# Performance work log

Hardware: AMD Instinct MI355X
Metric: run time of the kernel (lower is better)

## Reference

```python
import jax, jax.numpy as jnp
import numpy as np

N_NODES = 100000
N_EDGES = 1600000
F_IN = 64
HEADS = 4
F_OUT = 16
NEG_SLOPE = 0.2


def setup_inputs() -> dict:
    key = jax.random.key(0)
    k1, k2, k3, k4, k5 = jax.random.split(key, 5)
    x = jax.random.normal(k1, (N_NODES, F_IN), dtype=jnp.float32)
    edge_index = jax.random.randint(k2, (2, N_EDGES), 0, N_NODES, dtype=jnp.int64)
    # Glorot-ish scaled params
    W = jax.random.normal(k3, (HEADS, F_IN, F_OUT), dtype=jnp.float32) / np.sqrt(F_IN)
    a_src = jax.random.normal(k4, (HEADS, F_OUT), dtype=jnp.float32) / np.sqrt(F_OUT)
    a_dst = jax.random.normal(k5, (HEADS, F_OUT), dtype=jnp.float32) / np.sqrt(F_OUT)
    bias = jnp.zeros((HEADS * F_OUT,), dtype=jnp.float32)
    return {"x": x, "edge_index": edge_index, "W": W, "a_src": a_src,
            "a_dst": a_dst, "bias": bias}


def reference(x, edge_index, W, a_src, a_dst, bias):
    """Graph-attention conv (GAT-style) over a point-cloud graph.

    x: [N, F_in] node features; edge_index: [2, E] (src, dst);
    W: [H, F_in, F_out]; a_src/a_dst: [H, F_out]; bias: [H*F_out].
    Returns [N, H*F_out].
    """
    N = x.shape[0]
    src, dst = edge_index[0], edge_index[1]

    # Per-head linear projection: [N, H, F_out]
    h = jnp.einsum('nf,hfo->nho', x, W)

    # Per-node attention logits (decomposed GAT form): [N, H]
    logit_s = jnp.einsum('nho,ho->nh', h, a_src)
    logit_d = jnp.einsum('nho,ho->nh', h, a_dst)

    # Per-edge raw attention: [E, H]
    e = jax.nn.leaky_relu(logit_s[src] + logit_d[dst], negative_slope=NEG_SLOPE)

    # Segment softmax over incoming edges of each dst node
    m = jax.ops.segment_max(e, dst, num_segments=N)        # [N, H]
    m = jax.lax.stop_gradient(m)                           # softmax shift invariance
    e_exp = jnp.exp(e - m[dst])                            # [E, H]
    denom = jax.ops.segment_sum(e_exp, dst, num_segments=N)  # [N, H]
    alpha = e_exp / (denom[dst] + 1e-16)                   # [E, H]

    # Weighted message aggregation: scatter-add to dst
    msg = h[src] * alpha[:, :, None]                       # [E, H, F_out]
    out = jax.ops.segment_sum(msg, dst, num_segments=N)    # [N, H, F_out]

    return out.reshape(N, -1) + bias
```

## Files before the change

### kernel.cpp

```cpp
#include <hip/hip_runtime.h>

constexpr int N_NODES_C = 100000;
constexpr int N_EDGES_C = 1600000;
constexpr int F_IN_C = 64;
constexpr int HEADS_C = 4;
constexpr int F_OUT_C = 16;
constexpr float NEG_SLOPE_C = 0.2f;

constexpr int BUCK_SHIFT = 8;
constexpr int BUCK_NODES = 1 << BUCK_SHIFT;
constexpr int NBUCK = (N_NODES_C + BUCK_NODES - 1) / BUCK_NODES;
constexpr int BUCK_CAP = 5120;
constexpr int PART_BLOCKS = 256;
constexpr int EDGES_PER_PART_BLOCK = (N_EDGES_C + PART_BLOCKS - 1) / PART_BLOCKS;

typedef __attribute__((ext_vector_type(8))) short short8v;
typedef __attribute__((ext_vector_type(4))) float f32x4;

static __device__ __forceinline__ unsigned short f2bf(float f)
{
    const unsigned u = __float_as_uint(f);
    return (unsigned short)((u + 0x7FFF + ((u >> 16) & 1)) >> 16);
}
static __device__ __forceinline__ float bf2f(unsigned short b)
{
    return __uint_as_float(((unsigned)b) << 16);
}

__global__ __launch_bounds__(256) void k_prep(
    const float* __restrict__ W, const float* __restrict__ a_src,
    const float* __restrict__ a_dst, int* __restrict__ bucket_cursor,
    unsigned short* __restrict__ Bpack, unsigned short* __restrict__ Bpack2)
{
    __shared__ float sW[HEADS_C * F_IN_C * F_OUT_C];
    __shared__ float sA[2 * HEADS_C * F_OUT_C];
    const int t = threadIdx.x;
    for (int i = t; i < NBUCK; i += 256) bucket_cursor[i] = 0;
    for (int i = t; i < HEADS_C * F_IN_C * F_OUT_C; i += 256) sW[i] = W[i];
    if (t < HEADS_C * F_OUT_C) { sA[t] = a_src[t]; sA[64 + t] = a_dst[t]; }
    __syncthreads();

    for (int idx = t; idx < 4096; idx += 256) {
        const int j    = idx & 7;
        const int lane = (idx >> 3) & 63;
        const int nt   = (idx >> 9) & 3;
        const int kc   = (idx >> 11) & 1;
        const int col  = nt * 16 + (lane & 15);
        const int k    = kc * 32 + (lane >> 4) * 8 + j;
        Bpack[idx] = f2bf(sW[(col >> 4) * 1024 + k * 16 + (col & 15)]);
    }
    for (int idx = t; idx < 1024; idx += 256) {
        const int j    = idx & 7;
        const int lane = (idx >> 3) & 63;
        const int kc   = (idx >> 9) & 1;
        const int col  = lane & 15;
        const int k    = kc * 32 + (lane >> 4) * 8 + j;
        float v = 0.f;
        if (col < 8) {
            const int hd = col & 3;
            const float* wrow = &sW[hd * 1024 + k * 16];
            const float* av   = &sA[(col < 4 ? 0 : 64) + hd * 16];
            #pragma unroll
            for (int o = 0; o < 16; ++o) v = fmaf(wrow[o], av[o], v);
        }
        Bpack2[idx] = f2bf(v);
    }
}

__global__ __launch_bounds__(256) void k_project(
    const float* __restrict__ x, const unsigned short* __restrict__ Bpack,
    const unsigned short* __restrict__ Bpack2,
    unsigned short* __restrict__ h, float* __restrict__ ls, float* __restrict__ ld)
{
    const int wid  = threadIdx.x >> 6;
    const int lane = threadIdx.x & 63;
    const int node0 = (blockIdx.x * 4 + wid) * 16;
    const int colg = lane & 15;
    const int kg   = lane >> 4;

    const int rowc = min(node0 + colg, N_NODES_C - 1);
    short8v afrag[2];
    #pragma unroll
    for (int kc = 0; kc < 2; ++kc) {
        const float4* xp = (const float4*)&x[(size_t)rowc * 64 + kc * 32 + kg * 8];
        const float4 q0 = xp[0];
        const float4 q1 = xp[1];
        afrag[kc][0] = (short)f2bf(q0.x); afrag[kc][1] = (short)f2bf(q0.y);
        afrag[kc][2] = (short)f2bf(q0.z); afrag[kc][3] = (short)f2bf(q0.w);
        afrag[kc][4] = (short)f2bf(q1.x); afrag[kc][5] = (short)f2bf(q1.y);
        afrag[kc][6] = (short)f2bf(q1.z); afrag[kc][7] = (short)f2bf(q1.w);
    }

    f32x4 acc[4] = {{0.f,0.f,0.f,0.f},{0.f,0.f,0.f,0.f},
                    {0.f,0.f,0.f,0.f},{0.f,0.f,0.f,0.f}};
    f32x4 accL = {0.f,0.f,0.f,0.f};
    #pragma unroll
    for (int kc = 0; kc < 2; ++kc) {
        #pragma unroll
        for (int nt = 0; nt < 4; ++nt) {
            const short8v bfrag = *(const short8v*)&Bpack[((kc * 4 + nt) * 64 + lane) * 8];
            acc[nt] = __builtin_amdgcn_mfma_f32_16x16x32_bf16(afrag[kc], bfrag, acc[nt], 0, 0, 0);
        }
        const short8v bfrag2 = *(const short8v*)&Bpack2[(kc * 64 + lane) * 8];
        accL = __builtin_amdgcn_mfma_f32_16x16x32_bf16(afrag[kc], bfrag2, accL, 0, 0, 0);
    }

    #pragma unroll
    for (int nt = 0; nt < 4; ++nt) {
        #pragma unroll
        for (int i = 0; i < 4; ++i) {
            const int node = node0 + kg * 4 + i;
            if (node < N_NODES_C)
                h[(size_t)node * 64 + nt * 16 + colg] = f2bf(acc[nt][i]);
        }
    }
    #pragma unroll
    for (int i = 0; i < 4; ++i) {
        const int node = node0 + kg * 4 + i;
        if (node < N_NODES_C) {
            if (colg < 4)      ls[node * HEADS_C + colg]       = accL[i];
            else if (colg < 8) ld[node * HEADS_C + (colg - 4)] = accL[i];
        }
    }
}

__global__ __launch_bounds__(1024) void k_partition(
    const int* __restrict__ src, const int* __restrict__ dst,
    int* __restrict__ bucket_cursor, int* __restrict__ bucketed)
{
    __shared__ int cnt[NBUCK];
    __shared__ int base[NBUCK];
    __shared__ unsigned spack[EDGES_PER_PART_BLOCK];
    __shared__ unsigned short sbuck[EDGES_PER_PART_BLOCK];
    const int t = threadIdx.x;
    for (int i = t; i < NBUCK; i += 1024) cnt[i] = 0;
    __syncthreads();
    const int e0 = blockIdx.x * EDGES_PER_PART_BLOCK;
    const int nE = min(EDGES_PER_PART_BLOCK, N_EDGES_C - e0);
    for (int e = t; e < nE; e += 1024) {
        const int d = dst[e0 + e];
        const int b = d >> BUCK_SHIFT;
        spack[e] = (unsigned)src[e0 + e] | ((unsigned)(d & (BUCK_NODES - 1)) << 17);
        sbuck[e] = (unsigned short)b;
        atomicAdd(&cnt[b], 1);
    }
    __syncthreads();
    for (int i = t; i < NBUCK; i += 1024) {
        base[i] = atomicAdd(&bucket_cursor[i], cnt[i]);
        cnt[i] = 0;
    }
    __syncthreads();
    for (int e = t; e < nE; e += 1024) {
        const int b = sbuck[e];
        const int r = atomicAdd(&cnt[b], 1);
        const int p = base[b] + r;
        if (p < BUCK_CAP)
            bucketed[b * BUCK_CAP + p] = (int)spack[e];
    }
}

__global__ __launch_bounds__(256) void k_buildcsr(
    const int* __restrict__ bucket_cursor, const int* __restrict__ bucketed,
    int* __restrict__ csr_src, int* __restrict__ off, int* __restrict__ deg)
{
    __shared__ int hist[BUCK_NODES];
    __shared__ int pfx[BUCK_NODES];
    __shared__ int stageIn[BUCK_CAP];
    __shared__ int stageOut[BUCK_CAP];
    const int b = blockIdx.x;
    const int t = threadIdx.x;
    const int node0 = b * BUCK_NODES;
    const int nNodes = min(BUCK_NODES, N_NODES_C - node0);
    const int cnt = min(bucket_cursor[b], BUCK_CAP);
    const int* eb = &bucketed[(size_t)b * BUCK_CAP];

    hist[t] = 0;
    __syncthreads();
    for (int e = t; e < cnt; e += 256) {
        const int v = eb[e];
        stageIn[e] = v;
        atomicAdd(&hist[v >> 17], 1);
    }
    __syncthreads();
    const int myDeg = hist[t];
    pfx[t] = myDeg;
    __syncthreads();
    #pragma unroll
    for (int o = 1; o < BUCK_NODES; o <<= 1) {
        const int v = (t >= o) ? pfx[t - o] : 0;
        __syncthreads();
        pfx[t] += v;
        __syncthreads();
    }
    const int excl = pfx[t] - myDeg;
    if (t < nNodes) {
        deg[node0 + t] = myDeg;
        off[node0 + t] = b * BUCK_CAP + excl;
    }
    pfx[t] = excl;
    __syncthreads();
    for (int e = t; e < cnt; e += 256) {
        const int v = stageIn[e];
        const int r = atomicAdd(&pfx[v >> 17], 1);
        stageOut[r] = v & 0x1FFFF;
    }
    __syncthreads();
    int* outp = &csr_src[(size_t)b * BUCK_CAP];
    for (int e = t; e < cnt; e += 256) outp[e] = stageOut[e];
}

__global__ __launch_bounds__(256) void k_aggregate(
    const int* __restrict__ csr_src, const int* __restrict__ off,
    const int* __restrict__ deg, const float* __restrict__ ls,
    const float* __restrict__ ld, const unsigned short* __restrict__ h,
    const float* __restrict__ bias, float* __restrict__ out)
{
    const int wid  = threadIdx.x >> 6;
    const int lane = threadIdx.x & 63;
    const int d = blockIdx.x * 4 + wid;
    if (d >= N_NODES_C) return;
    const int hd = lane >> 4;
    const int jj = lane & 15;
    const int pb = (lane & 48) << 2;

    const int start = off[d];
    const int dg    = deg[d];
    const float ldv = ld[d * HEADS_C + hd];

    float acc  = 0.f;
    float denp = 0.f;

    if (dg <= 16) {
        int s_l = 0; float p_l = 0.f;
        if (jj < dg) {
            s_l = csr_src[start + jj];
            float v = ls[s_l * HEADS_C + hd] + ldv;
            v = (v > 0.f) ? v : v * NEG_SLOPE_C;
            p_l = __expf(v);
        }
        denp = p_l;
        unsigned short hv[16];
        #pragma unroll
        for (int j = 0; j < 16; ++j) {
            const int s_j = __builtin_amdgcn_readlane(s_l, j);
            hv[j] = h[(size_t)(unsigned)s_j * 64 + lane];
        }
        #pragma unroll
        for (int j = 0; j < 16; ++j) {
            const int pi = __builtin_amdgcn_ds_bpermute(pb + (j << 2), __float_as_int(p_l));
            acc = fmaf(__int_as_float(pi), bf2f(hv[j]), acc);
        }
    } else {
        for (int base = 0; base < dg; base += 32) {
            const int rem  = dg - base;
            const int nIn0 = min(16, rem);
            const int nIn1 = min(16, max(0, rem - 16));
            int s0 = 0, s1 = 0; float p0 = 0.f, p1 = 0.f;
            if (jj < nIn0) {
                s0 = csr_src[start + base + jj];
                float v = ls[s0 * HEADS_C + hd] + ldv;
                v = (v > 0.f) ? v : v * NEG_SLOPE_C;
                p0 = __expf(v);
            }
            if (jj < nIn1) {
                s1 = csr_src[start + base + 16 + jj];
                float v = ls[s1 * HEADS_C + hd] + ldv;
                v = (v > 0.f) ? v : v * NEG_SLOPE_C;
                p1 = __expf(v);
            }
            denp += p0 + p1;
            unsigned short hv0[16], hv1[16];
            #pragma unroll
            for (int j = 0; j < 16; ++j) {
                const int sj0 = __builtin_amdgcn_readlane(s0, j);
                hv0[j] = h[(size_t)(unsigned)sj0 * 64 + lane];
                const int sj1 = __builtin_amdgcn_readlane(s1, j);
                hv1[j] = h[(size_t)(unsigned)sj1 * 64 + lane];
            }
            #pragma unroll
            for (int j = 0; j < 16; ++j) {
                const int pi0 = __builtin_amdgcn_ds_bpermute(pb + (j << 2), __float_as_int(p0));
                acc = fmaf(__int_as_float(pi0), bf2f(hv0[j]), acc);
                const int pi1 = __builtin_amdgcn_ds_bpermute(pb + (j << 2), __float_as_int(p1));
                acc = fmaf(__int_as_float(pi1), bf2f(hv1[j]), acc);
            }
        }
    }
    #pragma unroll
    for (int o = 8; o >= 1; o >>= 1) denp += __shfl_xor(denp, o, 64);
    out[(size_t)d * 64 + lane] = acc / (denp + 1e-16f) + bias[lane];
}

extern "C" void kernel_launch(void* const* d_in, const int* in_sizes, int n_in,
                              void* d_out, int out_size, void* d_ws, size_t ws_size,
                              hipStream_t stream)
{
    const float* x     = (const float*)d_in[0];
    const int*   ei    = (const int*)d_in[1];
    const float* W     = (const float*)d_in[2];
    const float* a_src = (const float*)d_in[3];
    const float* a_dst = (const float*)d_in[4];
    const float* bias  = (const float*)d_in[5];
    float* out = (float*)d_out;

    float* ws   = (float*)d_ws;
    unsigned short* h = (unsigned short*)ws;
    float* ls   = (float*)(h + (size_t)N_NODES_C * 64);
    float* ld   = ls + (size_t)N_NODES_C * HEADS_C;
    int* bucket_cursor = (int*)(ld + (size_t)N_NODES_C * HEADS_C);
    int* deg     = bucket_cursor + NBUCK;
    int* off     = deg + N_NODES_C;
    int* bucketed = off + N_NODES_C;
    int* csr_src  = bucketed + (size_t)NBUCK * BUCK_CAP;
    unsigned short* Bpack  = (unsigned short*)(csr_src + (size_t)NBUCK * BUCK_CAP);
    unsigned short* Bpack2 = Bpack + 4096;

    const int* src = ei;
    const int* dst = ei + N_EDGES_C;

    k_prep<<<1, 256, 0, stream>>>(W, a_src, a_dst, bucket_cursor, Bpack, Bpack2);
    k_project<<<(N_NODES_C + 63) / 64, 256, 0, stream>>>(x, Bpack, Bpack2, h, ls, ld);
    k_partition<<<PART_BLOCKS, 1024, 0, stream>>>(src, dst, bucket_cursor, bucketed);
    k_buildcsr<<<NBUCK, 256, 0, stream>>>(bucket_cursor, bucketed, csr_src, off, deg);
    k_aggregate<<<(N_NODES_C + 3) / 4, 256, 0, stream>>>(csr_src, off, deg, ls, ld, h, bias, out);
}
```

Measured before the change: 100.0 us.

## Fuse per-bucket CSR build into aggregation kernel using shared-memory CSR

```diff
diff --git a/kernel.cpp b/kernel.cpp
--- a/kernel.cpp
+++ b/kernel.cpp
@@ -159,136 +159,125 @@
     }
 }
 
-__global__ __launch_bounds__(256) void k_buildcsr(
+__global__ __launch_bounds__(1024) void k_csr_aggregate(
     const int* __restrict__ bucket_cursor, const int* __restrict__ bucketed,
-    int* __restrict__ csr_src, int* __restrict__ off, int* __restrict__ deg)
+    const float* __restrict__ ls, const float* __restrict__ ld,
+    const unsigned short* __restrict__ h, const float* __restrict__ bias,
+    float* __restrict__ out)
 {
     __shared__ int hist[BUCK_NODES];
     __shared__ int pfx[BUCK_NODES];
-    __shared__ int stageIn[BUCK_CAP];
-    __shared__ int stageOut[BUCK_CAP];
+    __shared__ int stage[BUCK_CAP];
+    __shared__ int csr[BUCK_CAP];
     const int b = blockIdx.x;
     const int t = threadIdx.x;
     const int node0 = b * BUCK_NODES;
-    const int nNodes = min(BUCK_NODES, N_NODES_C - node0);
     const int cnt = min(bucket_cursor[b], BUCK_CAP);
     const int* eb = &bucketed[(size_t)b * BUCK_CAP];
 
-    hist[t] = 0;
-    __syncthreads();
-    for (int e = t; e < cnt; e += 256) {
+    if (t < BUCK_NODES) hist[t] = 0;
+    __syncthreads();
+    for (int e = t; e < cnt; e += 1024) {
         const int v = eb[e];
-        stageIn[e] = v;
+        stage[e] = v;
         atomicAdd(&hist[v >> 17], 1);
     }
     __syncthreads();
-    const int myDeg = hist[t];
-    pfx[t] = myDeg;
+    if (t < BUCK_NODES) pfx[t] = hist[t];
     __syncthreads();
     #pragma unroll
     for (int o = 1; o < BUCK_NODES; o <<= 1) {
-        const int v = (t >= o) ? pfx[t - o] : 0;
+        int v = 0;
+        if (t < BUCK_NODES && t >= o) v = pfx[t - o];
         __syncthreads();
-        pfx[t] += v;
+        if (t < BUCK_NODES) pfx[t] += v;
         __syncthreads();
     }
-    const int excl = pfx[t] - myDeg;
-    if (t < nNodes) {
-        deg[node0 + t] = myDeg;
-        off[node0 + t] = b * BUCK_CAP + excl;
-    }
-    pfx[t] = excl;
-    __syncthreads();
-    for (int e = t; e < cnt; e += 256) {
-        const int v = stageIn[e];
+    if (t < BUCK_NODES) pfx[t] -= hist[t];
+    __syncthreads();
+    for (int e = t; e < cnt; e += 1024) {
+        const int v = stage[e];
         const int r = atomicAdd(&pfx[v >> 17], 1);
-        stageOut[r] = v & 0x1FFFF;
-    }
-    __syncthreads();
-    int* outp = &csr_src[(size_t)b * BUCK_CAP];
-    for (int e = t; e < cnt; e += 256) outp[e] = stageOut[e];
-}
-
-__global__ __launch_bounds__(256) void k_aggregate(
-    const int* __restrict__ csr_src, const int* __restrict__ off,
-    const int* __restrict__ deg, const float* __restrict__ ls,
-    const float* __restrict__ ld, const unsigned short* __restrict__ h,
-    const float* __restrict__ bias, float* __restrict__ out)
-{
-    const int wid  = threadIdx.x >> 6;
-    const int lane = threadIdx.x & 63;
-    const int d = blockIdx.x * 4 + wid;
-    if (d >= N_NODES_C) return;
+        csr[r] = v & 0x1FFFF;
+    }
+    __syncthreads();
+
+    const int wv   = t >> 6;
+    const int lane = t & 63;
     const int hd = lane >> 4;
     const int jj = lane & 15;
     const int pb = (lane & 48) << 2;
 
-    const int start = off[d];
-    const int dg    = deg[d];
-    const float ldv = ld[d * HEADS_C + hd];
-
-    float acc  = 0.f;
-    float denp = 0.f;
-
-    if (dg <= 16) {
-        int s_l = 0; float p_l = 0.f;
-        if (jj < dg) {
-            s_l = csr_src[start + jj];
-            float v = ls[s_l * HEADS_C + hd] + ldv;
-            v = (v > 0.f) ? v : v * NEG_SLOPE_C;
-            p_l = __expf(v);
-        }
-        denp = p_l;
-        unsigned short hv[16];
-        #pragma unroll
-        for (int j = 0; j < 16; ++j) {
-            const int s_j = __builtin_amdgcn_readlane(s_l, j);
-            hv[j] = h[(size_t)(unsigned)s_j * 64 + lane];
-        }
-        #pragma unroll
-        for (int j = 0; j < 16; ++j) {
-            const int pi = __builtin_amdgcn_ds_bpermute(pb + (j << 2), __float_as_int(p_l));
-            acc = fmaf(__int_as_float(pi), bf2f(hv[j]), acc);
-        }
-    } else {
-        for (int base = 0; base < dg; base += 32) {
-            const int rem  = dg - base;
-            const int nIn0 = min(16, rem);
-            const int nIn1 = min(16, max(0, rem - 16));
-            int s0 = 0, s1 = 0; float p0 = 0.f, p1 = 0.f;
-            if (jj < nIn0) {
-                s0 = csr_src[start + base + jj];
-                float v = ls[s0 * HEADS_C + hd] + ldv;
+    for (int ln = wv; ln < BUCK_NODES; ln += 16) {
+        const int d = node0 + ln;
+        if (d >= N_NODES_C) continue;
+        const int dg    = hist[ln];
+        const int start = pfx[ln] - dg;
+        const float ldv = ld[d * HEADS_C + hd];
+
+        float acc  = 0.f;
+        float denp = 0.f;
+
+        if (dg <= 16) {
+            int s_l = 0; float p_l = 0.f;
+            if (jj < dg) {
+                s_l = csr[start + jj];
+                float v = ls[s_l * HEADS_C + hd] + ldv;
                 v = (v > 0.f) ? v : v * NEG_SLOPE_C;
-                p0 = __expf(v);
+                p_l = __expf(v);
             }
-            if (jj < nIn1) {
-                s1 = csr_src[start + base + 16 + jj];
-                float v = ls[s1 * HEADS_C + hd] + ldv;
-                v = (v > 0.f) ? v : v * NEG_SLOPE_C;
-                p1 = __expf(v);
-            }
-            denp += p0 + p1;
-            unsigned short hv0[16], hv1[16];
+            denp = p_l;
+            unsigned short hv[16];
             #pragma unroll
             for (int j = 0; j < 16; ++j) {
-                const int sj0 = __builtin_amdgcn_readlane(s0, j);
-                hv0[j] = h[(size_t)(unsigned)sj0 * 64 + lane];
-                const int sj1 = __builtin_amdgcn_readlane(s1, j);
-                hv1[j] = h[(size_t)(unsigned)sj1 * 64 + lane];
+                const int s_j = __builtin_amdgcn_readlane(s_l, j);
+                hv[j] = h[(size_t)(unsigned)s_j * 64 + lane];
             }
             #pragma unroll
             for (int j = 0; j < 16; ++j) {
-                const int pi0 = __builtin_amdgcn_ds_bpermute(pb + (j << 2), __float_as_int(p0));
-                acc = fmaf(__int_as_float(pi0), bf2f(hv0[j]), acc);
-                const int pi1 = __builtin_amdgcn_ds_bpermute(pb + (j << 2), __float_as_int(p1));
-                acc = fmaf(__int_as_float(pi1), bf2f(hv1[j]), acc);
+                const int pi = __builtin_amdgcn_ds_bpermute(pb + (j << 2), __float_as_int(p_l));
+                acc = fmaf(__int_as_float(pi), bf2f(hv[j]), acc);
             }
-        }
-    }
-    #pragma unroll
-    for (int o = 8; o >= 1; o >>= 1) denp += __shfl_xor(denp, o, 64);
-    out[(size_t)d * 64 + lane] = acc / (denp + 1e-16f) + bias[lane];
+        } else {
+            for (int base = 0; base < dg; base += 32) {
+                const int rem  = dg - base;
+                const int nIn0 = min(16, rem);
+                const int nIn1 = min(16, max(0, rem - 16));
+                int s0 = 0, s1 = 0; float p0 = 0.f, p1 = 0.f;
+                if (jj < nIn0) {
+                    s0 = csr[start + base + jj];
+                    float v = ls[s0 * HEADS_C + hd] + ldv;
+                    v = (v > 0.f) ? v : v * NEG_SLOPE_C;
+                    p0 = __expf(v);
+                }
+                if (jj < nIn1) {
+                    s1 = csr[start + base + 16 + jj];
+                    float v = ls[s1 * HEADS_C + hd] + ldv;
+                    v = (v > 0.f) ? v : v * NEG_SLOPE_C;
+                    p1 = __expf(v);
+                }
+                denp += p0 + p1;
+                unsigned short hv0[16], hv1[16];
+                #pragma unroll
+                for (int j = 0; j < 16; ++j) {
+                    const int sj0 = __builtin_amdgcn_readlane(s0, j);
+                    hv0[j] = h[(size_t)(unsigned)sj0 * 64 + lane];
+                    const int sj1 = __builtin_amdgcn_readlane(s1, j);
+                    hv1[j] = h[(size_t)(unsigned)sj1 * 64 + lane];
+                }
+                #pragma unroll
+                for (int j = 0; j < 16; ++j) {
+                    const int pi0 = __builtin_amdgcn_ds_bpermute(pb + (j << 2), __float_as_int(p0));
+                    acc = fmaf(__int_as_float(pi0), bf2f(hv0[j]), acc);
+                    const int pi1 = __builtin_amdgcn_ds_bpermute(pb + (j << 2), __float_as_int(p1));
+                    acc = fmaf(__int_as_float(pi1), bf2f(hv1[j]), acc);
+                }
+            }
+        }
+        #pragma unroll
+        for (int o = 8; o >= 1; o >>= 1) denp += __shfl_xor(denp, o, 64);
+        out[(size_t)d * 64 + lane] = acc / (denp + 1e-16f) + bias[lane];
+    }
 }
 
 extern "C" void kernel_launch(void* const* d_in, const int* in_sizes, int n_in,
@@ -308,11 +297,8 @@
     float* ls   = (float*)(h + (size_t)N_NODES_C * 64);
     float* ld   = ls + (size_t)N_NODES_C * HEADS_C;
     int* bucket_cursor = (int*)(ld + (size_t)N_NODES_C * HEADS_C);
-    int* deg     = bucket_cursor + NBUCK;
-    int* off     = deg + N_NODES_C;
-    int* bucketed = off + N_NODES_C;
-    int* csr_src  = bucketed + (size_t)NBUCK * BUCK_CAP;
-    unsigned short* Bpack  = (unsigned short*)(csr_src + (size_t)NBUCK * BUCK_CAP);
+    int* bucketed = bucket_cursor + NBUCK;
+    unsigned short* Bpack  = (unsigned short*)(bucketed + (size_t)NBUCK * BUCK_CAP);
     unsigned short* Bpack2 = Bpack + 4096;
 
     const int* src = ei;
@@ -321,6 +307,5 @@
     k_prep<<<1, 256, 0, stream>>>(W, a_src, a_dst, bucket_cursor, Bpack, Bpack2);
     k_project<<<(N_NODES_C + 63) / 64, 256, 0, stream>>>(x, Bpack, Bpack2, h, ls, ld);
     k_partition<<<PART_BLOCKS, 1024, 0, stream>>>(src, dst, bucket_cursor, bucketed);
-    k_buildcsr<<<NBUCK, 256, 0, stream>>>(bucket_cursor, bucketed, csr_src, off, deg);
-    k_aggregate<<<(N_NODES_C + 3) / 4, 256, 0, stream>>>(csr_src, off, deg, ls, ld, h, bias, out);
-}
+    k_csr_aggregate<<<NBUCK, 1024, 0, stream>>>(bucket_cursor, bucketed, ls, ld, h, bias, out);
+}
```

Measured after the change: 111.0 us. +10.9%, slower.
